# Kernel tuning notes

Measured on AMD Instinct MI355X. Metric: run time of the kernel, lower is better.

Reference implementation:

```python
import jax, jax.numpy as jnp
import numpy as np


def setup_inputs() -> dict:
    key = jax.random.key(0)
    k1, k2 = jax.random.split(key)
    B, N, F, K = 8, 8192, 128, 512
    x = jax.random.normal(k1, (B, N, F), dtype=jnp.float32)
    cluster_centers = jax.random.normal(k2, (K, F), dtype=jnp.float32)
    return {"x": x, "cluster_centers": cluster_centers}


def reference(x, cluster_centers):
    # same math as sqrt(sum((x - c)^2)) without the [B,N,K,F] intermediate).
    x_sq = jnp.sum(x * x, axis=-1, keepdims=True)                 # [B, N, 1]
    c_sq = jnp.sum(cluster_centers * cluster_centers, axis=-1)    # [K]
    cross = jnp.einsum("bnf,kf->bnk", x, cluster_centers)         # [B, N, K]
    d2 = jnp.maximum(x_sq + c_sq[None, None, :] - 2.0 * cross, 0.0)
    distances = jnp.sqrt(d2)                                      # [B, N, K]
    associations = jax.nn.softmax(-distances, axis=-1)            # [B, N, K]
    output = jnp.einsum("bnk,kf->bnf", associations, cluster_centers)
    return output
```

## Files before the change

### kernel.cpp

```cpp
#include <hip/hip_runtime.h>
#include <hip/hip_bf16.h>

typedef short v8s __attribute__((ext_vector_type(8)));
typedef float v16f __attribute__((ext_vector_type(16)));
typedef unsigned v2u __attribute__((ext_vector_type(2)));

#define F_ 128
#define K_ 512
#define M_ 65536
#define CH_SH 17408
#define CB_OFF 9216

typedef __attribute__((address_space(1))) const char gch;
typedef __attribute__((address_space(3))) char lch;

__device__ __forceinline__ short f2bf(float f) {
    union { float f; unsigned u; } v; v.f = f;
    unsigned u = v.u;
    u = (u + 0x7FFFu + ((u >> 16) & 1u)) >> 16;
    return (short)u;
}
__device__ __forceinline__ float bf2f(short s) {
    union { float f; unsigned u; } v;
    v.u = ((unsigned)(unsigned short)s) << 16;
    return v.f;
}

#if __has_builtin(__builtin_amdgcn_permlane32_swap)
#define HAVE_PLS 1
#endif

__device__ __forceinline__ void pswap(unsigned &a, unsigned &b, int lane) {
#ifdef HAVE_PLS
    v2u r = __builtin_amdgcn_permlane32_swap(a, b, false, false);
    a = (unsigned)r.x; b = (unsigned)r.y;
#else
    unsigned sa = (unsigned)__shfl_xor((int)a, 32);
    unsigned sb = (unsigned)__shfl_xor((int)b, 32);
    if (lane & 32) a = sb; else b = sa;
#endif
}

__global__ void prep_kernel(const float* __restrict__ centers, short* __restrict__ G) {
    const int c = blockIdx.x;
    const int f = threadIdx.x;
    const int ch = c >> 6, c64 = c & 63;
    const size_t base = (size_t)ch * CH_SH;
    float v = centers[c * F_ + f];
    short b = f2bf(v);
    float vb = bf2f(b);
    { const int ks = f >> 4, h = (f >> 3) & 1, j = f & 7;
      G[base + (size_t)((ks * 2 + h) * 64 + c64) * 8 + j] = b; }
    { const int kap = c64 >> 4, hh = (c64 >> 3) & 1, jj = c64 & 7;
      G[base + CB_OFF + (size_t)((kap * 2 + hh) * F_ + f) * 8 + jj] = b; }
    float s = vb * vb;
    #pragma unroll
    for (int off = 1; off < 64; off <<= 1) s += __shfl_xor(s, off);
    __shared__ float part[2];
    if ((f & 63) == 0) part[f >> 6] = s;
    __syncthreads();
    if (f < 16) {
        const float csq = part[0] + part[1];
        const float chv = -0.5f * csq;
        const short vh = f2bf(chv);
        const short vl = f2bf(chv - bf2f(vh));
        const short val = (f == 0) ? vh : (f == 1) ? vl : (f == 2) ? (short)0x3F80 : (short)0;
        const int h2 = f >> 3, j2 = f & 7;
        G[base + (size_t)((16 + h2) * 64 + c64) * 8 + j2] = val;
    }
}

__device__ __forceinline__ void stage_chunk(const short* __restrict__ G, short* dst,
                                            int ch, int wave, int lane) {
    const char* src = (const char*)(G + (size_t)ch * CH_SH);
    lch* d = (lch*)dst;
    #pragma unroll
    for (int t = 0; t < 4; ++t) {
        const int g = t * 512 + wave * 64 + lane;
        __builtin_amdgcn_global_load_lds((gch*)(src + (size_t)g * 16),
                                         d + (size_t)(t * 512 + wave * 64) * 16, 16, 0, 0);
    }
    if (wave < 2) {
        const int g = 2048 + wave * 64 + lane;
        __builtin_amdgcn_global_load_lds((gch*)(src + (size_t)g * 16),
                                         d + (size_t)(2048 + wave * 64) * 16, 16, 0, 0);
    }
}

__global__ __launch_bounds__(512, 2) void cluster_kernel(
        const float* __restrict__ x, const short* __restrict__ G,
        float* __restrict__ out) {
    __shared__ __align__(16) short SB[3][CH_SH];
    const int tid = threadIdx.x;
    const int wave = tid >> 6, lane = tid & 63;
    const int h = lane >> 5, c32 = lane & 31;
    const int row0 = blockIdx.x * 256 + wave * 32;

    const float4* xr4 = (const float4*)(x + (size_t)(row0 + c32) * F_);
    float4 xl[16];
    #pragma unroll
    for (int ks = 0; ks < 8; ++ks) {
        xl[2 * ks]     = xr4[ks * 4 + h * 2];
        xl[2 * ks + 1] = xr4[ks * 4 + h * 2 + 1];
    }
    v8s Bx[9];
    float xs = 0.f;
    #pragma unroll
    for (int ks = 0; ks < 8; ++ks) {
        float vv[8] = {xl[2*ks].x, xl[2*ks].y, xl[2*ks].z, xl[2*ks].w,
                       xl[2*ks+1].x, xl[2*ks+1].y, xl[2*ks+1].z, xl[2*ks+1].w};
        v8s fr;
        #pragma unroll
        for (int j = 0; j < 8; ++j) {
            short bb = f2bf(vv[j]);
            fr[j] = bb;
            float r = bf2f(bb);
            xs += r * r;
        }
        Bx[ks] = fr;
    }
    xs += __shfl_xor(xs, 32);
    {
        const float xh = -0.5f * xs;
        const short sxh = f2bf(xh);
        const short sxl = f2bf(xh - bf2f(sxh));
        v8s e = (v8s){0, 0, 0, 0, 0, 0, 0, 0};
        if (h == 0) { e[0] = (short)0x3F80; e[1] = (short)0x3F80; e[2] = sxh; e[3] = sxl; }
        Bx[8] = e;
    }

    v16f Of[4];
    #pragma unroll
    for (int ft = 0; ft < 4; ++ft)
        #pragma unroll
        for (int e2 = 0; e2 < 16; ++e2) Of[ft][e2] = 0.f;
    float lden = 0.f;

    short* const SB0 = &SB[0][0];
    const int off = blockIdx.x & 7;
    stage_chunk(G, SB0, off, wave, lane);
    stage_chunk(G, SB0 + CH_SH, (off + 1) & 7, wave, lane);

    #pragma unroll 1
    for (int j = 0; j < 8; ++j) {
        __syncthreads();
        if (j < 6)
            stage_chunk(G, SB0 + (size_t)((j + 2) % 3) * CH_SH, (off + j + 2) & 7, wave, lane);
        const short* CbS = SB0 + (size_t)(j % 3) * CH_SH;
        const short* CTS = CbS + CB_OFF;

        v16f a0, a1;
        #pragma unroll
        for (int e2 = 0; e2 < 16; ++e2) { a0[e2] = 0.f; a1[e2] = 0.f; }
        {
            v8s f0a = *(const v8s*)&CbS[(size_t)((0 * 2 + h) * 64 + c32) * 8];
            v8s f1a = *(const v8s*)&CbS[(size_t)((0 * 2 + h) * 64 + 32 + c32) * 8];
            v8s f0b = *(const v8s*)&CbS[(size_t)((1 * 2 + h) * 64 + c32) * 8];
            v8s f1b = *(const v8s*)&CbS[(size_t)((1 * 2 + h) * 64 + 32 + c32) * 8];
            #pragma unroll
            for (int ks = 0; ks < 9; ++ks) {
                v8s c0 = f0a, c1 = f1a;
                f0a = f0b; f1a = f1b;
                if (ks < 7) {
                    f0b = *(const v8s*)&CbS[(size_t)(((ks + 2) * 2 + h) * 64 + c32) * 8];
                    f1b = *(const v8s*)&CbS[(size_t)(((ks + 2) * 2 + h) * 64 + 32 + c32) * 8];
                }
                a0 = __builtin_amdgcn_mfma_f32_32x32x16_bf16(c0, Bx[ks], a0, 0, 0, 0);
                a1 = __builtin_amdgcn_mfma_f32_32x32x16_bf16(c1, Bx[ks], a1, 0, 0, 0);
            }
        }

        #pragma unroll
        for (int ct = 0; ct < 2; ++ct) {
            v8s cf[8];
            #pragma unroll
            for (int kp = 0; kp < 2; ++kp)
                #pragma unroll
                for (int ft = 0; ft < 4; ++ft)
                    cf[kp * 4 + ft] = *(const v8s*)
                        &CTS[(size_t)(((ct * 2 + kp) * 2 + h) * F_ + ft * 32 + c32) * 8];
            const v16f acc = ct ? a1 : a0;
            unsigned U[8];
            #pragma unroll
            for (int t = 0; t < 8; ++t) {
                const float d20 = fmaxf(-2.0f * acc[2 * t], 0.f);
                const float d21 = fmaxf(-2.0f * acc[2 * t + 1], 0.f);
                const float p0 = __expf(-__builtin_amdgcn_sqrtf(d20));
                const float p1 = __expf(-__builtin_amdgcn_sqrtf(d21));
                union { __hip_bfloat162 hh; unsigned u; } cv;
                cv.hh = __float22bfloat162_rn(make_float2(p0, p1));
                U[t] = cv.u;
                lden += __uint_as_float(cv.u << 16);
                lden += __uint_as_float(cv.u & 0xffff0000u);
            }
            #pragma unroll
            for (int kp = 0; kp < 2; ++kp) {
                unsigned s0 = U[4 * kp],     s2 = U[4 * kp + 2];
                unsigned s1 = U[4 * kp + 1], s3 = U[4 * kp + 3];
                pswap(s0, s2, lane);
                pswap(s1, s3, lane);
                union { v8s v; unsigned u[4]; } pf;
                pf.u[0] = s0; pf.u[1] = s1; pf.u[2] = s2; pf.u[3] = s3;
                #pragma unroll
                for (int ft = 0; ft < 4; ++ft)
                    Of[ft] = __builtin_amdgcn_mfma_f32_32x32x16_bf16(pf.v, cf[kp * 4 + ft], Of[ft], 0, 0, 0);
            }
        }
    }

    lden += __shfl_xor(lden, 32);
    const float inv = 1.0f / lden;
    float invr[16];
    #pragma unroll
    for (int r = 0; r < 16; ++r)
        invr[r] = __shfl(inv, (r & 3) + 8 * (r >> 2) + 4 * h);
    #pragma unroll
    for (int ft = 0; ft < 4; ++ft)
        #pragma unroll
        for (int r = 0; r < 16; ++r) {
            const int xrow = (r & 3) + 8 * (r >> 2) + 4 * h;
            out[(size_t)(row0 + xrow) * F_ + ft * 32 + c32] = Of[ft][r] * invr[r];
        }
}

extern "C" void kernel_launch(void* const* d_in, const int* in_sizes, int n_in,
                              void* d_out, int out_size, void* d_ws, size_t ws_size,
                              hipStream_t stream) {
    const float* x       = (const float*)d_in[0];
    const float* centers = (const float*)d_in[1];
    float* out = (float*)d_out;
    short* G = (short*)d_ws;
    prep_kernel<<<K_, F_, 0, stream>>>(centers, G);
    cluster_kernel<<<M_ / 256, 512, 0, stream>>>(x, G, out);
}
```

Before: 103.2 us.

## Keep all center fragments resident in LDS, read transposed centers from global

Splits the workspace into a distance-GEMM block and a transposed-center block. The distance-GEMM block for all 8 chunks is staged into LDS once at kernel start, which removes the triple-buffered per-chunk staging and the per-iteration block barriers. The transposed center fragments for the second GEMM are now read straight from global/L2 and prefetched before use, and each wave starts on a different chunk. The softmax exponent is folded into one scale plus exp2 (log2e pre-squared into the constant). This trades per-iteration syncs for a larger LDS footprint (144KB per block, which may limit occupancy to one block per CU) and global-latency loads inside the loop.

```diff
diff --git a/kernel.cpp b/kernel.cpp
--- a/kernel.cpp
+++ b/kernel.cpp
@@ -8,8 +8,9 @@
 #define F_ 128
 #define K_ 512
 #define M_ 65536
-#define CH_SH 17408
-#define CB_OFF 9216
+#define CB_CH 9216
+#define CT_CH 8192
+#define CT_BASE 73728
 
 typedef __attribute__((address_space(1))) const char gch;
 typedef __attribute__((address_space(3))) char lch;
@@ -45,14 +46,13 @@
     const int c = blockIdx.x;
     const int f = threadIdx.x;
     const int ch = c >> 6, c64 = c & 63;
-    const size_t base = (size_t)ch * CH_SH;
     float v = centers[c * F_ + f];
     short b = f2bf(v);
     float vb = bf2f(b);
     { const int ks = f >> 4, h = (f >> 3) & 1, j = f & 7;
-      G[base + (size_t)((ks * 2 + h) * 64 + c64) * 8 + j] = b; }
+      G[(size_t)ch * CB_CH + (size_t)((ks * 2 + h) * 64 + c64) * 8 + j] = b; }
     { const int kap = c64 >> 4, hh = (c64 >> 3) & 1, jj = c64 & 7;
-      G[base + CB_OFF + (size_t)((kap * 2 + hh) * F_ + f) * 8 + jj] = b; }
+      G[CT_BASE + (size_t)ch * CT_CH + (size_t)((kap * 2 + hh) * F_ + f) * 8 + jj] = b; }
     float s = vb * vb;
     #pragma unroll
     for (int off = 1; off < 64; off <<= 1) s += __shfl_xor(s, off);
@@ -66,35 +66,28 @@
         const short vl = f2bf(chv - bf2f(vh));
         const short val = (f == 0) ? vh : (f == 1) ? vl : (f == 2) ? (short)0x3F80 : (short)0;
         const int h2 = f >> 3, j2 = f & 7;
-        G[base + (size_t)((16 + h2) * 64 + c64) * 8 + j2] = val;
-    }
-}
-
-__device__ __forceinline__ void stage_chunk(const short* __restrict__ G, short* dst,
-                                            int ch, int wave, int lane) {
-    const char* src = (const char*)(G + (size_t)ch * CH_SH);
-    lch* d = (lch*)dst;
-    #pragma unroll
-    for (int t = 0; t < 4; ++t) {
-        const int g = t * 512 + wave * 64 + lane;
-        __builtin_amdgcn_global_load_lds((gch*)(src + (size_t)g * 16),
-                                         d + (size_t)(t * 512 + wave * 64) * 16, 16, 0, 0);
-    }
-    if (wave < 2) {
-        const int g = 2048 + wave * 64 + lane;
-        __builtin_amdgcn_global_load_lds((gch*)(src + (size_t)g * 16),
-                                         d + (size_t)(2048 + wave * 64) * 16, 16, 0, 0);
+        G[(size_t)ch * CB_CH + (size_t)((16 + h2) * 64 + c64) * 8 + j2] = val;
     }
 }
 
 __global__ __launch_bounds__(512, 2) void cluster_kernel(
         const float* __restrict__ x, const short* __restrict__ G,
         float* __restrict__ out) {
-    __shared__ __align__(16) short SB[3][CH_SH];
+    __shared__ __align__(16) short SBall[CT_BASE];
     const int tid = threadIdx.x;
     const int wave = tid >> 6, lane = tid & 63;
     const int h = lane >> 5, c32 = lane & 31;
     const int row0 = blockIdx.x * 256 + wave * 32;
+
+    {
+        lch* d = (lch*)SBall;
+        #pragma unroll
+        for (int t = 0; t < 18; ++t) {
+            const int gbase = t * 512 + wave * 64;
+            __builtin_amdgcn_global_load_lds((gch*)((const char*)G + (size_t)(gbase + lane) * 16),
+                                             d + (size_t)gbase * 16, 16, 0, 0);
+        }
+    }
 
     const float4* xr4 = (const float4*)(x + (size_t)(row0 + c32) * F_);
     float4 xl[16];
@@ -136,18 +129,21 @@
         for (int e2 = 0; e2 < 16; ++e2) Of[ft][e2] = 0.f;
     float lden = 0.f;
 
-    short* const SB0 = &SB[0][0];
-    const int off = blockIdx.x & 7;
-    stage_chunk(G, SB0, off, wave, lane);
-    stage_chunk(G, SB0 + CH_SH, (off + 1) & 7, wave, lane);
+    __syncthreads();
 
     #pragma unroll 1
     for (int j = 0; j < 8; ++j) {
-        __syncthreads();
-        if (j < 6)
-            stage_chunk(G, SB0 + (size_t)((j + 2) % 3) * CH_SH, (off + j + 2) & 7, wave, lane);
-        const short* CbS = SB0 + (size_t)(j % 3) * CH_SH;
-        const short* CTS = CbS + CB_OFF;
+        const int ch = (wave + blockIdx.x + j) & 7;
+        const short* CbS = SBall + (size_t)ch * CB_CH;
+        const short* CTGc = G + CT_BASE + (size_t)ch * CT_CH;
+
+        v8s cf0[8];
+        #pragma unroll
+        for (int kp = 0; kp < 2; ++kp)
+            #pragma unroll
+            for (int ft = 0; ft < 4; ++ft)
+                cf0[kp * 4 + ft] = *(const v8s*)
+                    &CTGc[(size_t)((kp * 2 + h) * F_ + ft * 32 + c32) * 8];
 
         v16f a0, a1;
         #pragma unroll
@@ -170,41 +166,61 @@
             }
         }
 
-        #pragma unroll
-        for (int ct = 0; ct < 2; ++ct) {
-            v8s cf[8];
-            #pragma unroll
-            for (int kp = 0; kp < 2; ++kp)
-                #pragma unroll
-                for (int ft = 0; ft < 4; ++ft)
-                    cf[kp * 4 + ft] = *(const v8s*)
-                        &CTS[(size_t)(((ct * 2 + kp) * 2 + h) * F_ + ft * 32 + c32) * 8];
-            const v16f acc = ct ? a1 : a0;
-            unsigned U[8];
-            #pragma unroll
-            for (int t = 0; t < 8; ++t) {
-                const float d20 = fmaxf(-2.0f * acc[2 * t], 0.f);
-                const float d21 = fmaxf(-2.0f * acc[2 * t + 1], 0.f);
-                const float p0 = __expf(-__builtin_amdgcn_sqrtf(d20));
-                const float p1 = __expf(-__builtin_amdgcn_sqrtf(d21));
-                union { __hip_bfloat162 hh; unsigned u; } cv;
-                cv.hh = __float22bfloat162_rn(make_float2(p0, p1));
-                U[t] = cv.u;
-                lden += __uint_as_float(cv.u << 16);
-                lden += __uint_as_float(cv.u & 0xffff0000u);
-            }
-            #pragma unroll
-            for (int kp = 0; kp < 2; ++kp) {
-                unsigned s0 = U[4 * kp],     s2 = U[4 * kp + 2];
-                unsigned s1 = U[4 * kp + 1], s3 = U[4 * kp + 3];
-                pswap(s0, s2, lane);
-                pswap(s1, s3, lane);
-                union { v8s v; unsigned u[4]; } pf;
-                pf.u[0] = s0; pf.u[1] = s1; pf.u[2] = s2; pf.u[3] = s3;
-                #pragma unroll
-                for (int ft = 0; ft < 4; ++ft)
-                    Of[ft] = __builtin_amdgcn_mfma_f32_32x32x16_bf16(pf.v, cf[kp * 4 + ft], Of[ft], 0, 0, 0);
-            }
+        unsigned U[8];
+        #pragma unroll
+        for (int t = 0; t < 8; ++t) {
+            const float s20 = fmaxf(-4.16273796f * a0[2 * t], 0.f);
+            const float s21 = fmaxf(-4.16273796f * a0[2 * t + 1], 0.f);
+            const float p0 = __builtin_amdgcn_exp2f(-__builtin_amdgcn_sqrtf(s20));
+            const float p1 = __builtin_amdgcn_exp2f(-__builtin_amdgcn_sqrtf(s21));
+            union { __hip_bfloat162 hh; unsigned u; } cv;
+            cv.hh = __float22bfloat162_rn(make_float2(p0, p1));
+            U[t] = cv.u;
+            lden += __uint_as_float(cv.u << 16);
+            lden += __uint_as_float(cv.u & 0xffff0000u);
+        }
+        v8s cf1[8];
+        #pragma unroll
+        for (int kp = 0; kp < 2; ++kp)
+            #pragma unroll
+            for (int ft = 0; ft < 4; ++ft)
+                cf1[kp * 4 + ft] = *(const v8s*)
+                    &CTGc[(size_t)(((2 + kp) * 2 + h) * F_ + ft * 32 + c32) * 8];
+        #pragma unroll
+        for (int kp = 0; kp < 2; ++kp) {
+            unsigned s0 = U[4 * kp],     s2 = U[4 * kp + 2];
+            unsigned s1 = U[4 * kp + 1], s3 = U[4 * kp + 3];
+            pswap(s0, s2, lane);
+            pswap(s1, s3, lane);
+            union { v8s v; unsigned u[4]; } pf;
+            pf.u[0] = s0; pf.u[1] = s1; pf.u[2] = s2; pf.u[3] = s3;
+            #pragma unroll
+            for (int ft = 0; ft < 4; ++ft)
+                Of[ft] = __builtin_amdgcn_mfma_f32_32x32x16_bf16(pf.v, cf0[kp * 4 + ft], Of[ft], 0, 0, 0);
+        }
+        #pragma unroll
+        for (int t = 0; t < 8; ++t) {
+            const float s20 = fmaxf(-4.16273796f * a1[2 * t], 0.f);
+            const float s21 = fmaxf(-4.16273796f * a1[2 * t + 1], 0.f);
+            const float p0 = __builtin_amdgcn_exp2f(-__builtin_amdgcn_sqrtf(s20));
+            const float p1 = __builtin_amdgcn_exp2f(-__builtin_amdgcn_sqrtf(s21));
+            union { __hip_bfloat162 hh; unsigned u; } cv;
+            cv.hh = __float22bfloat162_rn(make_float2(p0, p1));
+            U[t] = cv.u;
+            lden += __uint_as_float(cv.u << 16);
+            lden += __uint_as_float(cv.u & 0xffff0000u);
+        }
+        #pragma unroll
+        for (int kp = 0; kp < 2; ++kp) {
+            unsigned s0 = U[4 * kp],     s2 = U[4 * kp + 2];
+            unsigned s1 = U[4 * kp + 1], s3 = U[4 * kp + 3];
+            pswap(s0, s2, lane);
+            pswap(s1, s3, lane);
+            union { v8s v; unsigned u[4]; } pf;
+            pf.u[0] = s0; pf.u[1] = s1; pf.u[2] = s2; pf.u[3] = s3;
+            #pragma unroll
+            for (int ft = 0; ft < 4; ++ft)
+                Of[ft] = __builtin_amdgcn_mfma_f32_32x32x16_bf16(pf.v, cf1[kp * 4 + ft], Of[ft], 0, 0, 0);
         }
     }
 
```

Result: slower. 106.1 us (+2.8%).
